# Performance work log

Hardware: AMD Instinct MI355X
Metric: run time of the kernel (lower is better)

## Reference

```python
import jax, jax.numpy as jnp
import numpy as np

N = 50000
S = 32           # n_sample
D_IN = 256
D_OUT = 128
ALPHA = 0.2      # leakyrelu negative slope


def setup_inputs() -> dict:
    key = jax.random.key(0)
    k1, k2, k3, k4 = jax.random.split(key, 4)
    x = jax.random.normal(k1, (N, D_IN), dtype=jnp.float32)
    neibs = jax.random.randint(k2, (N, S), 0, N, dtype=jnp.int64)
    # xavier_uniform with gain=1.414
    limW = 1.414 * np.sqrt(6.0 / (D_IN + D_OUT))
    W = jax.random.uniform(k3, (D_IN, D_OUT), dtype=jnp.float32, minval=-limW, maxval=limW)
    lima = 1.414 * np.sqrt(6.0 / (2 * D_OUT + 1))
    a = jax.random.uniform(k4, (2 * D_OUT, 1), dtype=jnp.float32, minval=-lima, maxval=lima)
    return {"x": x, "neibs": neibs, "W": W, "a": a}


def reference(x, neibs, W, a):
    # x: [N, D_in], neibs: [N, S] int, W: [D_in, D_out], a: [2*D_out, 1]
    xw = x @ W                                  # [N, D_out]
    xn = xw[neibs]                              # [N, S, D_out] gathered neighbor feats
    # a_input @ a == xw @ a[:D_out] + xn @ a[D_out:]  (avoid materializing concat)
    a_self = a[:D_OUT, 0]                       # [D_out]
    a_neib = a[D_OUT:, 0]                       # [D_out]
    e = (xw @ a_self)[:, None] + jnp.einsum('nsd,d->ns', xn, a_neib)  # [N, S]
    e = jnp.where(e > 0, e, ALPHA * e)          # leakyrelu
    attention = jax.nn.softmax(e, axis=1)       # [N, S]  (dropout skipped: eval mode)
    h_prime = jnp.einsum('ns,nsd->nd', attention, xn)                # [N, D_out]
    output = jnp.concatenate([xw, h_prime], axis=1)                  # concat=True
    return jax.nn.elu(output)
```

## Files before the change

kernel.cpp:

```cpp
#include <hip/hip_runtime.h>
#include <math.h>

#define N_NODES 50000
#define S_NEIB 32
#define D_IN 256
#define D_OUT 128
#define ALPHA 0.2f
#define QSCALE 12.0f
#define QINV   (127.0f / QSCALE)
#define QDEQ   (QSCALE / 127.0f)

typedef __attribute__((ext_vector_type(8))) short bf16x8;
typedef __attribute__((ext_vector_type(4))) float f32x4;

__device__ __forceinline__ float elu_f(float v) {
    return v > 0.f ? v : (expf(v) - 1.f);
}

__device__ __forceinline__ unsigned short f2bf(float f) {
    unsigned u = __builtin_bit_cast(unsigned, f);
    u += 0x7fffu + ((u >> 16) & 1u);
    return (unsigned short)(u >> 16);
}

__device__ __forceinline__ bf16x8 pack_bf16x8(float4 v0, float4 v1) {
    bf16x8 r;
    r[0] = (short)f2bf(v0.x); r[1] = (short)f2bf(v0.y);
    r[2] = (short)f2bf(v0.z); r[3] = (short)f2bf(v0.w);
    r[4] = (short)f2bf(v1.x); r[5] = (short)f2bf(v1.y);
    r[6] = (short)f2bf(v1.z); r[7] = (short)f2bf(v1.w);
    return r;
}

__device__ __forceinline__ signed char q8(float v) {
    float qf = fminf(fmaxf(rintf(v * QINV), -127.f), 127.f);
    return (signed char)(int)qf;
}

__global__ __launch_bounds__(256) void pack_w_kernel(
    const float* __restrict__ W, unsigned short* __restrict__ Wp)
{
    int tid = blockIdx.x * 256 + threadIdx.x;
    int j  = tid & 7;
    int t  = (tid >> 3) & 15;
    int kb = (tid >> 7) & 31;
    int c  = tid >> 12;
    Wp[tid] = f2bf(W[(kb * 8 + j) * D_OUT + c * 16 + t]);
}

__global__ __launch_bounds__(256, 4) void gemm_score_kernel(
    const float* __restrict__ x, const unsigned short* __restrict__ Wp,
    const float* __restrict__ a, signed char* __restrict__ xq,
    float* __restrict__ s_self, float* __restrict__ s_neib)
{
    __shared__ unsigned short xb[32 * 256];
    __shared__ float ps[2][4][32];

    const int tid  = threadIdx.x;
    const int lane = tid & 63;
    const int wave = tid >> 6;
    const int q    = lane >> 4;
    const int t    = lane & 15;
    const int colW = wave * 32;
    const int r0   = blockIdx.x * 32;

    const bf16x8* Wp8 = (const bf16x8*)Wp;

    bf16x8 bv[8][2];
    #pragma unroll
    for (int kc = 0; kc < 8; ++kc)
        #pragma unroll
        for (int nt = 0; nt < 2; ++nt)
            bv[kc][nt] = Wp8[((wave * 2 + nt) * 32 + kc * 4 + q) * 16 + t];

    #pragma unroll
    for (int s = 0; s < 4; ++s) {
        int g   = tid + 256 * s;
        int row = g >> 5;
        int c   = g & 31;
        const float* xp = x + (size_t)min(r0 + row, N_NODES - 1) * D_IN + c * 8;
        float4 v0 = *(const float4*)xp;
        float4 v1 = *(const float4*)(xp + 4);
        *(bf16x8*)((char*)xb + row * 512 + ((c ^ (row & 7)) * 16)) =
            pack_bf16x8(v0, v1);
    }
    __syncthreads();

    f32x4 acc[2][2];
    #pragma unroll
    for (int mt = 0; mt < 2; ++mt)
        #pragma unroll
        for (int nt = 0; nt < 2; ++nt)
            acc[mt][nt] = (f32x4){0.f, 0.f, 0.f, 0.f};

    #pragma unroll
    for (int kc = 0; kc < 8; ++kc) {
        bf16x8 afrag[2];
        #pragma unroll
        for (int mt = 0; mt < 2; ++mt) {
            int row = mt * 16 + t;
            afrag[mt] = *(const bf16x8*)((const char*)xb + row * 512
                        + (((kc * 4 + q) ^ (t & 7)) * 16));
        }
        #pragma unroll
        for (int mt = 0; mt < 2; ++mt)
            #pragma unroll
            for (int nt = 0; nt < 2; ++nt)
                acc[mt][nt] = __builtin_amdgcn_mfma_f32_16x16x32_bf16(
                    afrag[mt], bv[kc][nt], acc[mt][nt], 0, 0, 0);
    }

    const float as0 = a[colW + t],         as1 = a[colW + 16 + t];
    const float an0 = a[D_OUT + colW + t], an1 = a[D_OUT + colW + 16 + t];
    #pragma unroll
    for (int mt = 0; mt < 2; ++mt) {
        #pragma unroll
        for (int r = 0; r < 4; ++r) {
            float vs = acc[mt][0][r] * as0 + acc[mt][1][r] * as1;
            float vn = acc[mt][0][r] * an0 + acc[mt][1][r] * an1;
            #pragma unroll
            for (int d = 8; d >= 1; d >>= 1) {
                vs += __shfl_xor(vs, d);
                vn += __shfl_xor(vn, d);
            }
            if (t == 0) {
                int row = mt * 16 + q * 4 + r;
                ps[0][wave][row] = vs;
                ps[1][wave][row] = vn;
            }
        }
    }
    __syncthreads();
    if (tid < 32 && r0 + tid < N_NODES) {
        s_self[r0 + tid] = ps[0][0][tid] + ps[0][1][tid] + ps[0][2][tid] + ps[0][3][tid];
        s_neib[r0 + tid] = ps[1][0][tid] + ps[1][1][tid] + ps[1][2][tid] + ps[1][3][tid];
    }

    #pragma unroll
    for (int mt = 0; mt < 2; ++mt) {
        #pragma unroll
        for (int r = 0; r < 4; ++r) {
            int g = r0 + mt * 16 + q * 4 + r;
            if (g < N_NODES) {
                #pragma unroll
                for (int nt = 0; nt < 2; ++nt)
                    xq[(size_t)g * D_OUT + colW + nt * 16 + t] = q8(acc[mt][nt][r]);
            }
        }
    }
}

__global__ __launch_bounds__(256, 4) void aggregate_kernel(
    const int* __restrict__ neibs, const signed char* __restrict__ xq,
    const float* __restrict__ s_self, const float* __restrict__ s_neib,
    float* __restrict__ out)
{
    const int lane  = threadIdx.x & 63;
    const int wavei = threadIdx.x >> 6;
    const int hl    = lane & 15;
    const int grp   = lane & 48;
    const int node  = blockIdx.x * 16 + wavei * 4 + (lane >> 4);

    const int ebase = node * S_NEIB + hl;
    const int idxA  = neibs[ebase];
    const int idxB  = neibs[ebase + 16];

    const signed char* colp = xq + 8 * hl;

    uint2 own = *(const uint2*)(colp + (size_t)node * D_OUT);
    uint2 v[32];
    #pragma unroll
    for (int i = 0; i < 16; ++i) {
        int j = __shfl(idxA, grp + i);
        v[i] = *(const uint2*)(colp + (size_t)j * D_OUT);
    }
    #pragma unroll
    for (int i = 0; i < 16; ++i) {
        int j = __shfl(idxB, grp + i);
        v[16 + i] = *(const uint2*)(colp + (size_t)j * D_OUT);
    }

    const float ss = s_self[node];
    float eA = ss + s_neib[idxA];
    float eB = ss + s_neib[idxB];
    eA = eA > 0.f ? eA : ALPHA * eA;
    eB = eB > 0.f ? eB : ALPHA * eB;

    float m = fmaxf(eA, eB);
    #pragma unroll
    for (int d = 8; d >= 1; d >>= 1) m = fmaxf(m, __shfl_xor(m, d));
    float pA = __expf(eA - m), pB = __expf(eB - m);
    float s = pA + pB;
    #pragma unroll
    for (int d = 8; d >= 1; d >>= 1) s += __shfl_xor(s, d);
    const float inv = QDEQ / s;
    const float wA = pA * inv, wB = pB * inv;

    float ac[8] = {0.f, 0.f, 0.f, 0.f, 0.f, 0.f, 0.f, 0.f};
    #pragma unroll
    for (int i = 0; i < 32; ++i) {
        float w = __shfl(i < 16 ? wA : wB, grp + (i & 15));
        unsigned lo = v[i].x, hi = v[i].y;
        ac[0] = fmaf(w, (float)((int)(lo << 24) >> 24), ac[0]);
        ac[1] = fmaf(w, (float)((int)(lo << 16) >> 24), ac[1]);
        ac[2] = fmaf(w, (float)((int)(lo <<  8) >> 24), ac[2]);
        ac[3] = fmaf(w, (float)((int)lo >> 24),         ac[3]);
        ac[4] = fmaf(w, (float)((int)(hi << 24) >> 24), ac[4]);
        ac[5] = fmaf(w, (float)((int)(hi << 16) >> 24), ac[5]);
        ac[6] = fmaf(w, (float)((int)(hi <<  8) >> 24), ac[6]);
        ac[7] = fmaf(w, (float)((int)hi >> 24),         ac[7]);
    }

    float* orow = out + (size_t)node * (2 * D_OUT);

    f32x4 o1a, o1b;
    o1a.x = elu_f((float)((int)(own.x << 24) >> 24) * QDEQ);
    o1a.y = elu_f((float)((int)(own.x << 16) >> 24) * QDEQ);
    o1a.z = elu_f((float)((int)(own.x <<  8) >> 24) * QDEQ);
    o1a.w = elu_f((float)((int)own.x >> 24)         * QDEQ);
    o1b.x = elu_f((float)((int)(own.y << 24) >> 24) * QDEQ);
    o1b.y = elu_f((float)((int)(own.y << 16) >> 24) * QDEQ);
    o1b.z = elu_f((float)((int)(own.y <<  8) >> 24) * QDEQ);
    o1b.w = elu_f((float)((int)own.y >> 24)         * QDEQ);
    __builtin_nontemporal_store(o1a, (f32x4*)(orow + 8 * hl));
    __builtin_nontemporal_store(o1b, (f32x4*)(orow + 8 * hl + 4));

    f32x4 o2a, o2b;
    o2a.x = elu_f(ac[0]); o2a.y = elu_f(ac[1]);
    o2a.z = elu_f(ac[2]); o2a.w = elu_f(ac[3]);
    o2b.x = elu_f(ac[4]); o2b.y = elu_f(ac[5]);
    o2b.z = elu_f(ac[6]); o2b.w = elu_f(ac[7]);
    __builtin_nontemporal_store(o2a, (f32x4*)(orow + D_OUT + 8 * hl));
    __builtin_nontemporal_store(o2b, (f32x4*)(orow + D_OUT + 8 * hl + 4));
}

extern "C" void kernel_launch(void* const* d_in, const int* in_sizes, int n_in,
                              void* d_out, int out_size, void* d_ws, size_t ws_size,
                              hipStream_t stream) {
    const float* x     = (const float*)d_in[0];
    const int*   neibs = (const int*)  d_in[1];
    const float* W     = (const float*)d_in[2];
    const float* a     = (const float*)d_in[3];
    float* out = (float*)d_out;

    signed char* xq    = (signed char*)d_ws;
    float* s_self      = (float*)(xq + (size_t)N_NODES * D_OUT);
    float* s_neib      = s_self + N_NODES;
    unsigned short* Wp = (unsigned short*)(s_neib + N_NODES);

    pack_w_kernel<<<128, 256, 0, stream>>>(W, Wp);
    gemm_score_kernel<<<(N_NODES + 31) / 32, 256, 0, stream>>>(
        x, Wp, a, xq, s_self, s_neib);
    aggregate_kernel<<<N_NODES / 16, 256, 0, stream>>>(
        neibs, xq, s_self, s_neib, out);
}
```

Before: 137.4 us.

## Split aggregation into two column-half passes with 4-byte gathers

The aggregation kernel now handles only 64 of the 128 quantized feature columns per launch, and it is launched twice with a column offset. Each lane gathers 4 bytes per neighbour instead of 8, which halves the register footprint of the gathered values and may raise occupancy. In exchange, neighbour indices, scores and softmax are read and recomputed twice, and each gather touches a 64-byte segment of the row instead of the full 128 bytes, which adds memory transactions.

```diff
diff --git a/kernel.cpp b/kernel.cpp
--- a/kernel.cpp
+++ b/kernel.cpp
@@ -153,7 +153,7 @@
 __global__ __launch_bounds__(256, 4) void aggregate_kernel(
     const int* __restrict__ neibs, const signed char* __restrict__ xq,
     const float* __restrict__ s_self, const float* __restrict__ s_neib,
-    float* __restrict__ out)
+    float* __restrict__ out, int col0)
 {
     const int lane  = threadIdx.x & 63;
     const int wavei = threadIdx.x >> 6;
@@ -165,19 +165,19 @@
     const int idxA  = neibs[ebase];
     const int idxB  = neibs[ebase + 16];
 
-    const signed char* colp = xq + 8 * hl;
-
-    uint2 own = *(const uint2*)(colp + (size_t)node * D_OUT);
-    uint2 v[32];
+    const signed char* colp = xq + col0 + 4 * hl;
+
+    unsigned own = *(const unsigned*)(colp + (size_t)node * D_OUT);
+    unsigned v[32];
     #pragma unroll
     for (int i = 0; i < 16; ++i) {
         int j = __shfl(idxA, grp + i);
-        v[i] = *(const uint2*)(colp + (size_t)j * D_OUT);
+        v[i] = *(const unsigned*)(colp + (size_t)j * D_OUT);
     }
     #pragma unroll
     for (int i = 0; i < 16; ++i) {
         int j = __shfl(idxB, grp + i);
-        v[16 + i] = *(const uint2*)(colp + (size_t)j * D_OUT);
+        v[16 + i] = *(const unsigned*)(colp + (size_t)j * D_OUT);
     }
 
     const float ss = s_self[node];
@@ -196,42 +196,32 @@
     const float inv = QDEQ / s;
     const float wA = pA * inv, wB = pB * inv;
 
-    float ac[8] = {0.f, 0.f, 0.f, 0.f, 0.f, 0.f, 0.f, 0.f};
+    float a0 = 0.f, a1 = 0.f, a2 = 0.f, a3 = 0.f;
     #pragma unroll
     for (int i = 0; i < 32; ++i) {
         float w = __shfl(i < 16 ? wA : wB, grp + (i & 15));
-        unsigned lo = v[i].x, hi = v[i].y;
-        ac[0] = fmaf(w, (float)((int)(lo << 24) >> 24), ac[0]);
-        ac[1] = fmaf(w, (float)((int)(lo << 16) >> 24), ac[1]);
-        ac[2] = fmaf(w, (float)((int)(lo <<  8) >> 24), ac[2]);
-        ac[3] = fmaf(w, (float)((int)lo >> 24),         ac[3]);
-        ac[4] = fmaf(w, (float)((int)(hi << 24) >> 24), ac[4]);
-        ac[5] = fmaf(w, (float)((int)(hi << 16) >> 24), ac[5]);
-        ac[6] = fmaf(w, (float)((int)(hi <<  8) >> 24), ac[6]);
-        ac[7] = fmaf(w, (float)((int)hi >> 24),         ac[7]);
-    }
-
-    float* orow = out + (size_t)node * (2 * D_OUT);
-
-    f32x4 o1a, o1b;
-    o1a.x = elu_f((float)((int)(own.x << 24) >> 24) * QDEQ);
-    o1a.y = elu_f((float)((int)(own.x << 16) >> 24) * QDEQ);
-    o1a.z = elu_f((float)((int)(own.x <<  8) >> 24) * QDEQ);
-    o1a.w = elu_f((float)((int)own.x >> 24)         * QDEQ);
-    o1b.x = elu_f((float)((int)(own.y << 24) >> 24) * QDEQ);
-    o1b.y = elu_f((float)((int)(own.y << 16) >> 24) * QDEQ);
-    o1b.z = elu_f((float)((int)(own.y <<  8) >> 24) * QDEQ);
-    o1b.w = elu_f((float)((int)own.y >> 24)         * QDEQ);
-    __builtin_nontemporal_store(o1a, (f32x4*)(orow + 8 * hl));
-    __builtin_nontemporal_store(o1b, (f32x4*)(orow + 8 * hl + 4));
-
-    f32x4 o2a, o2b;
-    o2a.x = elu_f(ac[0]); o2a.y = elu_f(ac[1]);
-    o2a.z = elu_f(ac[2]); o2a.w = elu_f(ac[3]);
-    o2b.x = elu_f(ac[4]); o2b.y = elu_f(ac[5]);
-    o2b.z = elu_f(ac[6]); o2b.w = elu_f(ac[7]);
-    __builtin_nontemporal_store(o2a, (f32x4*)(orow + D_OUT + 8 * hl));
-    __builtin_nontemporal_store(o2b, (f32x4*)(orow + D_OUT + 8 * hl + 4));
+        unsigned vv = v[i];
+        a0 = fmaf(w, (float)((int)(vv << 24) >> 24), a0);
+        a1 = fmaf(w, (float)((int)(vv << 16) >> 24), a1);
+        a2 = fmaf(w, (float)((int)(vv <<  8) >> 24), a2);
+        a3 = fmaf(w, (float)((int)vv >> 24),         a3);
+    }
+
+    float* orow = out + (size_t)node * (2 * D_OUT) + col0 + 4 * hl;
+
+    f32x4 o1;
+    o1.x = elu_f((float)((int)(own << 24) >> 24) * QDEQ);
+    o1.y = elu_f((float)((int)(own << 16) >> 24) * QDEQ);
+    o1.z = elu_f((float)((int)(own <<  8) >> 24) * QDEQ);
+    o1.w = elu_f((float)((int)own >> 24)         * QDEQ);
+    __builtin_nontemporal_store(o1, (f32x4*)orow);
+
+    f32x4 o2;
+    o2.x = elu_f(a0);
+    o2.y = elu_f(a1);
+    o2.z = elu_f(a2);
+    o2.w = elu_f(a3);
+    __builtin_nontemporal_store(o2, (f32x4*)(orow + D_OUT));
 }
 
 extern "C" void kernel_launch(void* const* d_in, const int* in_sizes, int n_in,
@@ -252,5 +242,7 @@
     gemm_score_kernel<<<(N_NODES + 31) / 32, 256, 0, stream>>>(
         x, Wp, a, xq, s_self, s_neib);
     aggregate_kernel<<<N_NODES / 16, 256, 0, stream>>>(
-        neibs, xq, s_self, s_neib, out);
-}
+        neibs, xq, s_self, s_neib, out, 0);
+    aggregate_kernel<<<N_NODES / 16, 256, 0, stream>>>(
+        neibs, xq, s_self, s_neib, out, 64);
+}
```

Measured after the change: 151.2 us. 10.1% more time.
